# Optimization experiments

Hardware: AMD Instinct MI355X
Metric: run time of the kernel (lower is better)

The kernel has to match this reference:

```python
import jax, jax.numpy as jnp
import numpy as np

IC, OC, ID, OD = 1152, 10, 8, 16   # input_caps, output_caps, input_dim, output_dim
N_ITER = 5
THRESHOLD = 1e-05
EPS = 1e-20


def setup_inputs() -> dict:
    key = jax.random.key(0)
    k1, k2 = jax.random.split(key)
    x = jax.random.uniform(k1, (32, IC, ID), dtype=jnp.float32)
    # replicate CapsLayer.__init__ + norm_weights(): uniform(0,1), normalize over
    # output_caps dim, clamp to threshold, renormalize
    w = jax.random.uniform(k2, (IC, OC, ID, OD), dtype=jnp.float32)
    w = w / (w.sum(axis=1, keepdims=True) + EPS)
    w = jnp.clip(w, THRESHOLD, None)
    w = w / (w.sum(axis=1, keepdims=True) + EPS)
    return {"x": x, "weights": w}


def nnmf_sbs(inp, weights):
    # inp: [B, ic, id], weights: [ic, oc, id, od] -> out: [B, ic, oc, od]
    B = inp.shape[0]
    out0 = jnp.full((B, IC, OC, OD), 1.0 / OD, dtype=inp.dtype)

    def body(out, _):
        h_w = out[:, :, :, None, :] * weights[None]          # [B,ic,oc,id,od]
        h_w = h_w / (h_w.sum(-1, keepdims=True) + EPS)       # normalize over od
        h_w = (h_w * inp[:, :, None, :, None]).sum(-2)       # reduce id -> [B,ic,oc,od]
        out = h_w / (h_w.sum(-1, keepdims=True) + EPS)       # normalize over od
        return out, None

    out, _ = jax.lax.scan(body, out0, None, length=N_ITER)
    return out


def reference(x, weights):
    x = x / (x.sum(-1, keepdims=True) + EPS)                 # normalize over input_dim
    h = nnmf_sbs(x, weights)                                 # [B,ic,oc,od]
    # reconstruct = (h.unsqueeze(-2) * weights).sum(-1) -> [B,ic,oc,id]
    reconstruct = jnp.einsum('bicd,iced->bice', h, weights)
    alpha = jnp.einsum('bice,bie->bic', reconstruct, x)      # [B,ic,oc]
    alpha = alpha / (alpha.sum(-1, keepdims=True) + EPS)     # normalize over oc
    return jnp.einsum('bicd,bic->bcd', h, alpha)             # sum over ic -> [B,oc,od]
```

## Files before the change

### kernel.cpp

```cpp
#include <hip/hip_runtime.h>

#define B_   32
#define ICN  1152
#define OCN  10
#define IDN  8
#define ODN  16
#define ODH  8
#define NIT  5
#define EPS  1e-20f
#define OUTN (B_ * OCN * ODN)
#define BGRP 11
#define NBLK (BGRP * ICN)

__global__ __launch_bounds__(64, 4) void caps_main(
    const float* __restrict__ xg, const float* __restrict__ wg,
    float* __restrict__ ws, float* __restrict__ outg, int atomic_out) {
  const int l = threadIdx.x;
  const int bid = blockIdx.x;
  const int ic = bid % ICN;
  const int bgrp = bid / ICN;
  const int grp = l / 20;
  const int q = l % 20;
  const int oc = q >> 1;
  const int half = q & 1;
  const int b = bgrp * 3 + grp;
  const bool valid = (grp < 3) && (b < B_);
  const int bb = (b < B_) ? b : (B_ - 1);

  float wr[IDN][ODH];
  {
    const float* wp = wg + ((size_t)ic * OCN + oc) * (IDN * ODN) + half * ODH;
#pragma unroll
    for (int id = 0; id < IDN; ++id) {
      const float4 v0 = *(const float4*)(wp + id * ODN);
      const float4 v1 = *(const float4*)(wp + id * ODN + 4);
      wr[id][0] = v0.x; wr[id][1] = v0.y; wr[id][2] = v0.z; wr[id][3] = v0.w;
      wr[id][4] = v1.x; wr[id][5] = v1.y; wr[id][6] = v1.z; wr[id][7] = v1.w;
    }
  }

  float xn[IDN];
  {
    const float* xp = xg + ((size_t)bb * ICN + ic) * IDN;
    const float4 a0 = ((const float4*)xp)[0];
    const float4 a1 = ((const float4*)xp)[1];
    xn[0] = a0.x; xn[1] = a0.y; xn[2] = a0.z; xn[3] = a0.w;
    xn[4] = a1.x; xn[5] = a1.y; xn[6] = a1.z; xn[7] = a1.w;
    float s = 0.f;
#pragma unroll
    for (int i = 0; i < IDN; ++i) s += xn[i];
    const float r = __builtin_amdgcn_rcpf(s + EPS);
#pragma unroll
    for (int i = 0; i < IDN; ++i) xn[i] *= r;
  }

  float h[ODH];
#pragma unroll
  for (int k = 0; k < ODH; ++k) h[k] = 1.0f / ODN;

  for (int it = 0; it < NIT; ++it) {
    float hacc[ODH];
#pragma unroll
    for (int k = 0; k < ODH; ++k) hacc[k] = 0.f;
#pragma unroll
    for (int id = 0; id < IDN; ++id) {
      float pd = 0.f;
#pragma unroll
      for (int k = 0; k < ODH; ++k) pd = fmaf(h[k], wr[id][k], pd);
      const float den = pd + __shfl_xor(pd, 1, 64);
      const float tc = xn[id] * __builtin_amdgcn_rcpf(den + EPS);
#pragma unroll
      for (int k = 0; k < ODH; ++k) hacc[k] = fmaf(wr[id][k], tc, hacc[k]);
    }
    float ps = 0.f;
#pragma unroll
    for (int k = 0; k < ODH; ++k) { h[k] *= hacc[k]; ps += h[k]; }
    const float hs = ps + __shfl_xor(ps, 1, 64);
    const float r = __builtin_amdgcn_rcpf(hs + EPS);
#pragma unroll
    for (int k = 0; k < ODH; ++k) h[k] *= r;
  }

  float ap = 0.f;
#pragma unroll
  for (int id = 0; id < IDN; ++id) {
    float rec = 0.f;
#pragma unroll
    for (int k = 0; k < ODH; ++k) rec = fmaf(h[k], wr[id][k], rec);
    ap = fmaf(rec, xn[id], ap);
  }
  const float af = ap + __shfl_xor(ap, 1, 64);
  float asum = 0.f;
  const int gbase = grp * 20;
#pragma unroll
  for (int k = 0; k < OCN; ++k) asum += __shfl(af, gbase + 2 * k, 64);
  const float an = af * __builtin_amdgcn_rcpf(asum + EPS);

  float o[ODH];
#pragma unroll
  for (int k = 0; k < ODH; ++k) o[k] = h[k] * an;

  if (valid) {
    if (!atomic_out) {
      float* dst = ws + (size_t)ic * OUTN + (bb * OCN + oc) * ODN + half * ODH;
      float4 v0, v1;
      v0.x = o[0]; v0.y = o[1]; v0.z = o[2]; v0.w = o[3];
      v1.x = o[4]; v1.y = o[5]; v1.z = o[6]; v1.w = o[7];
      ((float4*)dst)[0] = v0;
      ((float4*)dst)[1] = v1;
    } else {
      const int base = (bb * OCN + oc) * ODN + half * ODH;
#pragma unroll
      for (int k = 0; k < ODH; ++k) atomicAdd(outg + base + k, o[k]);
    }
  }
}

#define RSPLIT 32
#define RROWS  (ICN / RSPLIT)
__global__ void caps_reduce(const float* __restrict__ ws, float* __restrict__ outg) {
  const int j = blockIdx.x * 256 + threadIdx.x;
  const int r0 = blockIdx.y * RROWS;
  float s = 0.f;
#pragma unroll
  for (int r = 0; r < RROWS; ++r) s += ws[(size_t)(r0 + r) * OUTN + j];
  atomicAdd(outg + j, s);
}

extern "C" void kernel_launch(void* const* d_in, const int* in_sizes, int n_in,
                              void* d_out, int out_size, void* d_ws, size_t ws_size,
                              hipStream_t stream) {
  const float* x = (const float*)d_in[0];
  const float* w = (const float*)d_in[1];
  float* out = (float*)d_out;
  float* ws = (float*)d_ws;

  hipMemsetAsync(out, 0, OUTN * sizeof(float), stream);

  const size_t need = (size_t)ICN * OUTN * sizeof(float);

  if (ws_size >= need) {
    caps_main<<<NBLK, 64, 0, stream>>>(x, w, ws, out, 0);
    caps_reduce<<<dim3(OUTN / 256, RSPLIT), 256, 0, stream>>>(ws, out);
  } else {
    caps_main<<<NBLK, 64, 0, stream>>>(x, w, nullptr, out, 1);
  }
}
```

Measured before the change: 90.87 us.

## Loop several input capsules per block and accumulate in registers with atomics

```diff
diff --git a/kernel.cpp b/kernel.cpp
--- a/kernel.cpp
+++ b/kernel.cpp
@@ -9,122 +9,141 @@
 #define NIT  5
 #define EPS  1e-20f
 #define OUTN (B_ * OCN * ODN)
+#define KI   6
+#define NICB (ICN / KI)
 #define BGRP 11
-#define NBLK (BGRP * ICN)
+#define NBLK (NICB * BGRP)
 
-__global__ __launch_bounds__(64, 4) void caps_main(
+__device__ __forceinline__ float lane_swap1(float x) {
+  int i = __builtin_bit_cast(int, x);
+  int r = __builtin_amdgcn_mov_dpp(i, 0xB1, 0xF, 0xF, false);
+  return __builtin_bit_cast(float, r);
+}
+
+__device__ __forceinline__ float2 f2_fma(const float2 a, const float2 b, const float2 c) {
+  float2 r;
+  r.x = fmaf(a.x, b.x, c.x);
+  r.y = fmaf(a.y, b.y, c.y);
+  return r;
+}
+__device__ __forceinline__ float2 f2_mul(const float2 a, const float2 b) {
+  float2 r; r.x = a.x * b.x; r.y = a.y * b.y; return r;
+}
+
+__global__ __launch_bounds__(64, 2) void caps_main(
     const float* __restrict__ xg, const float* __restrict__ wg,
-    float* __restrict__ ws, float* __restrict__ outg, int atomic_out) {
+    float* __restrict__ outg) {
   const int l = threadIdx.x;
   const int bid = blockIdx.x;
-  const int ic = bid % ICN;
-  const int bgrp = bid / ICN;
+  const int icb = bid % NICB;
+  const int bgrp = bid / NICB;
   const int grp = l / 20;
   const int q = l % 20;
   const int oc = q >> 1;
   const int half = q & 1;
   const int b = bgrp * 3 + grp;
   const bool valid = (grp < 3) && (b < B_);
-  const int bb = (b < B_) ? b : (B_ - 1);
+  const int bb = (b < B_) ? b : 0;
 
-  float wr[IDN][ODH];
-  {
-    const float* wp = wg + ((size_t)ic * OCN + oc) * (IDN * ODN) + half * ODH;
+  float2 acc[4];
+#pragma unroll
+  for (int j = 0; j < 4; ++j) acc[j] = make_float2(0.f, 0.f);
+
+  for (int k = 0; k < KI; ++k) {
+    const int ic = icb * KI + k;
+
+    float2 w2[IDN][4];
+    {
+      const float* wp = wg + ((size_t)ic * OCN + oc) * (IDN * ODN) + half * ODH;
+#pragma unroll
+      for (int id = 0; id < IDN; ++id) {
+        const float4 v0 = *(const float4*)(wp + id * ODN);
+        const float4 v1 = *(const float4*)(wp + id * ODN + 4);
+        w2[id][0] = make_float2(v0.x, v0.y);
+        w2[id][1] = make_float2(v0.z, v0.w);
+        w2[id][2] = make_float2(v1.x, v1.y);
+        w2[id][3] = make_float2(v1.z, v1.w);
+      }
+    }
+
+    float xn[IDN];
+    {
+      const float* xp = xg + ((size_t)bb * ICN + ic) * IDN;
+      const float4 a0 = ((const float4*)xp)[0];
+      const float4 a1 = ((const float4*)xp)[1];
+      xn[0] = a0.x; xn[1] = a0.y; xn[2] = a0.z; xn[3] = a0.w;
+      xn[4] = a1.x; xn[5] = a1.y; xn[6] = a1.z; xn[7] = a1.w;
+      float s = 0.f;
+#pragma unroll
+      for (int i = 0; i < IDN; ++i) s += xn[i];
+      const float r = __builtin_amdgcn_rcpf(s + EPS);
+#pragma unroll
+      for (int i = 0; i < IDN; ++i) xn[i] *= r;
+    }
+
+    float2 h2[4];
+#pragma unroll
+    for (int j = 0; j < 4; ++j) h2[j] = make_float2(1.f / ODN, 1.f / ODN);
+
+    for (int it = 0; it < NIT; ++it) {
+      float2 hacc[4];
+#pragma unroll
+      for (int j = 0; j < 4; ++j) hacc[j] = make_float2(0.f, 0.f);
+#pragma unroll
+      for (int id = 0; id < IDN; ++id) {
+        float2 d2 = f2_mul(h2[0], w2[id][0]);
+        d2 = f2_fma(h2[1], w2[id][1], d2);
+        d2 = f2_fma(h2[2], w2[id][2], d2);
+        d2 = f2_fma(h2[3], w2[id][3], d2);
+        const float pd = d2.x + d2.y;
+        const float den = pd + lane_swap1(pd);
+        const float tc = xn[id] * __builtin_amdgcn_rcpf(den + EPS);
+        const float2 t2 = make_float2(tc, tc);
+#pragma unroll
+        for (int j = 0; j < 4; ++j) hacc[j] = f2_fma(w2[id][j], t2, hacc[j]);
+      }
+      float2 s2 = make_float2(0.f, 0.f);
+#pragma unroll
+      for (int j = 0; j < 4; ++j) {
+        h2[j] = f2_mul(h2[j], hacc[j]);
+        s2.x += h2[j].x; s2.y += h2[j].y;
+      }
+      const float ps = s2.x + s2.y;
+      const float hs = ps + lane_swap1(ps);
+      const float r = __builtin_amdgcn_rcpf(hs + EPS);
+      const float2 r2 = make_float2(r, r);
+#pragma unroll
+      for (int j = 0; j < 4; ++j) h2[j] = f2_mul(h2[j], r2);
+    }
+
+    float ap = 0.f;
 #pragma unroll
     for (int id = 0; id < IDN; ++id) {
-      const float4 v0 = *(const float4*)(wp + id * ODN);
-      const float4 v1 = *(const float4*)(wp + id * ODN + 4);
-      wr[id][0] = v0.x; wr[id][1] = v0.y; wr[id][2] = v0.z; wr[id][3] = v0.w;
-      wr[id][4] = v1.x; wr[id][5] = v1.y; wr[id][6] = v1.z; wr[id][7] = v1.w;
+      float2 d2 = f2_mul(h2[0], w2[id][0]);
+      d2 = f2_fma(h2[1], w2[id][1], d2);
+      d2 = f2_fma(h2[2], w2[id][2], d2);
+      d2 = f2_fma(h2[3], w2[id][3], d2);
+      ap = fmaf(d2.x + d2.y, xn[id], ap);
+    }
+    const float af = ap + lane_swap1(ap);
+    float asum = 0.f;
+    const int gbase = grp * 20;
+#pragma unroll
+    for (int k2 = 0; k2 < OCN; ++k2) asum += __shfl(af, gbase + 2 * k2, 64);
+    const float an = af * __builtin_amdgcn_rcpf(asum + EPS);
+    const float2 an2 = make_float2(an, an);
+#pragma unroll
+    for (int j = 0; j < 4; ++j) acc[j] = f2_fma(h2[j], an2, acc[j]);
+  }
+
+  if (valid) {
+    float* dst = outg + (bb * OCN + oc) * ODN + half * ODH;
+#pragma unroll
+    for (int j = 0; j < 4; ++j) {
+      atomicAdd(dst + j * 2 + 0, acc[j].x);
+      atomicAdd(dst + j * 2 + 1, acc[j].y);
     }
   }
-
-  float xn[IDN];
-  {
-    const float* xp = xg + ((size_t)bb * ICN + ic) * IDN;
-    const float4 a0 = ((const float4*)xp)[0];
-    const float4 a1 = ((const float4*)xp)[1];
-    xn[0] = a0.x; xn[1] = a0.y; xn[2] = a0.z; xn[3] = a0.w;
-    xn[4] = a1.x; xn[5] = a1.y; xn[6] = a1.z; xn[7] = a1.w;
-    float s = 0.f;
-#pragma unroll
-    for (int i = 0; i < IDN; ++i) s += xn[i];
-    const float r = __builtin_amdgcn_rcpf(s + EPS);
-#pragma unroll
-    for (int i = 0; i < IDN; ++i) xn[i] *= r;
-  }
-
-  float h[ODH];
-#pragma unroll
-  for (int k = 0; k < ODH; ++k) h[k] = 1.0f / ODN;
-
-  for (int it = 0; it < NIT; ++it) {
-    float hacc[ODH];
-#pragma unroll
-    for (int k = 0; k < ODH; ++k) hacc[k] = 0.f;
-#pragma unroll
-    for (int id = 0; id < IDN; ++id) {
-      float pd = 0.f;
-#pragma unroll
-      for (int k = 0; k < ODH; ++k) pd = fmaf(h[k], wr[id][k], pd);
-      const float den = pd + __shfl_xor(pd, 1, 64);
-      const float tc = xn[id] * __builtin_amdgcn_rcpf(den + EPS);
-#pragma unroll
-      for (int k = 0; k < ODH; ++k) hacc[k] = fmaf(wr[id][k], tc, hacc[k]);
-    }
-    float ps = 0.f;
-#pragma unroll
-    for (int k = 0; k < ODH; ++k) { h[k] *= hacc[k]; ps += h[k]; }
-    const float hs = ps + __shfl_xor(ps, 1, 64);
-    const float r = __builtin_amdgcn_rcpf(hs + EPS);
-#pragma unroll
-    for (int k = 0; k < ODH; ++k) h[k] *= r;
-  }
-
-  float ap = 0.f;
-#pragma unroll
-  for (int id = 0; id < IDN; ++id) {
-    float rec = 0.f;
-#pragma unroll
-    for (int k = 0; k < ODH; ++k) rec = fmaf(h[k], wr[id][k], rec);
-    ap = fmaf(rec, xn[id], ap);
-  }
-  const float af = ap + __shfl_xor(ap, 1, 64);
-  float asum = 0.f;
-  const int gbase = grp * 20;
-#pragma unroll
-  for (int k = 0; k < OCN; ++k) asum += __shfl(af, gbase + 2 * k, 64);
-  const float an = af * __builtin_amdgcn_rcpf(asum + EPS);
-
-  float o[ODH];
-#pragma unroll
-  for (int k = 0; k < ODH; ++k) o[k] = h[k] * an;
-
-  if (valid) {
-    if (!atomic_out) {
-      float* dst = ws + (size_t)ic * OUTN + (bb * OCN + oc) * ODN + half * ODH;
-      float4 v0, v1;
-      v0.x = o[0]; v0.y = o[1]; v0.z = o[2]; v0.w = o[3];
-      v1.x = o[4]; v1.y = o[5]; v1.z = o[6]; v1.w = o[7];
-      ((float4*)dst)[0] = v0;
-      ((float4*)dst)[1] = v1;
-    } else {
-      const int base = (bb * OCN + oc) * ODN + half * ODH;
-#pragma unroll
-      for (int k = 0; k < ODH; ++k) atomicAdd(outg + base + k, o[k]);
-    }
-  }
-}
-
-#define RSPLIT 32
-#define RROWS  (ICN / RSPLIT)
-__global__ void caps_reduce(const float* __restrict__ ws, float* __restrict__ outg) {
-  const int j = blockIdx.x * 256 + threadIdx.x;
-  const int r0 = blockIdx.y * RROWS;
-  float s = 0.f;
-#pragma unroll
-  for (int r = 0; r < RROWS; ++r) s += ws[(size_t)(r0 + r) * OUTN + j];
-  atomicAdd(outg + j, s);
 }
 
 extern "C" void kernel_launch(void* const* d_in, const int* in_sizes, int n_in,
@@ -133,16 +152,7 @@
   const float* x = (const float*)d_in[0];
   const float* w = (const float*)d_in[1];
   float* out = (float*)d_out;
-  float* ws = (float*)d_ws;
 
   hipMemsetAsync(out, 0, OUTN * sizeof(float), stream);
-
-  const size_t need = (size_t)ICN * OUTN * sizeof(float);
-
-  if (ws_size >= need) {
-    caps_main<<<NBLK, 64, 0, stream>>>(x, w, ws, out, 0);
-    caps_reduce<<<dim3(OUTN / 256, RSPLIT), 256, 0, stream>>>(ws, out);
-  } else {
-    caps_main<<<NBLK, 64, 0, stream>>>(x, w, nullptr, out, 1);
-  }
+  caps_main<<<NBLK, 64, 0, stream>>>(x, w, out);
 }
```

After: 152.9 us. 68.3% more time.
